# Optimization experiments

Hardware: AMD Instinct MI355X
Metric: run time of the kernel (lower is better)

Reference implementation:

```python
import jax, jax.numpy as jnp
import numpy as np
from jax import lax

KERNEL_SIZE = 2  # init kwarg erode_kernel


def _min_filter_same(x, k):
    """Separable k x k min-filter (erosion) over the last two dims of NCHW x,
    SAME output size, out-of-bounds padded with +inf (matches cv2.erode's
    default border value, which never wins the min)."""
    inf = jnp.asarray(jnp.inf, x.dtype)
    # rows pass then cols pass; square min-filter is separable
    y = lax.reduce_window(x, inf, lax.min,
                          window_dimensions=(1, 1, k, 1),
                          window_strides=(1, 1, 1, 1),
                          padding='SAME')
    y = lax.reduce_window(y, inf, lax.min,
                          window_dimensions=(1, 1, 1, k),
                          window_strides=(1, 1, 1, 1),
                          padding='SAME')
    return y


def setup_inputs() -> dict:
    key = jax.random.key(0)
    x = jax.random.normal(key, (32, 3, 512, 512), dtype=jnp.float32)
    return {"x": x, "l": 1, "gpu": 0}


def reference(x, l, gpu):
    # iterations_times = 4 * (l + 2 - 1); erosion window grows by 2*iters
    iterations_times = 4 * (l + 1)
    k = KERNEL_SIZE + 2 * iterations_times  # 18 for l=1
    # original: tensor2pil(e * 0.5 + 0.5) -> cv2.erode -> pil2tensor ([0,1])
    # (uint8 quantization of the PIL round-trip is omitted; same min-filter math)
    y = x * 0.5 + 0.5
    y = _min_filter_same(y, k)
    return y
```

## Files before the change

### kernel.cpp

```cpp
#include <hip/hip_runtime.h>


#define IMG_H 512
#define IMG_W 512
#define RLO 8

__device__ __forceinline__ float finf() { return __int_as_float(0x7f800000); }


__global__ __launch_bounds__(256, 4)
void erode_fused_22187801051678(const float* __restrict__ in,
                                float* __restrict__ out) {
    __shared__ float B[32][145];
    __shared__ float Bo[32][129];

    const int tid = threadIdx.x;
    const int w0 = blockIdx.x * 128;
    const int h0 = blockIdx.y * 32;
    const size_t plane = (size_t)blockIdx.z * (IMG_H * IMG_W);

    for (int u = tid; u < 290; u += 256) {
        int col, seg;
        if (u < 145) { col = u;       seg = 0; }
        else         { col = u - 145; seg = 1; }
        const int gw  = w0 - RLO + col;
        const bool wok = (unsigned)gw < (unsigned)IMG_W;
        const int ghb = h0 - RLO + seg * 16;

        float x[33];
#pragma unroll
        for (int i = 0; i < 33; ++i) {
            const int gh = ghb + i;
            float v = finf();
            if (wok && (unsigned)gh < (unsigned)IMG_H)
                v = in[plane + (size_t)gh * IMG_W + gw];
            x[i] = v;
        }
        float p[32];
#pragma unroll
        for (int i = 0; i < 32; ++i) p[i] = fminf(x[i], x[i + 1]);
        float q[30];
#pragma unroll
        for (int i = 0; i < 30; ++i) q[i] = fminf(p[i], p[i + 2]);
#pragma unroll
        for (int j = 0; j < 16; ++j) {
            float m = fminf(fminf(q[j], q[j + 4]), fminf(q[j + 8], q[j + 12]));
            m = fminf(m, p[j + 16]);
            B[seg * 16 + j][col] = m;
        }
    }
    __syncthreads();

    {
        const int r  = tid & 31;
        const int c8 = tid >> 5;
        float y[33];
#pragma unroll
        for (int i = 0; i < 33; ++i) y[i] = B[r][c8 * 16 + i];
        float p[32];
#pragma unroll
        for (int i = 0; i < 32; ++i) p[i] = fminf(y[i], y[i + 1]);
        float q[30];
#pragma unroll
        for (int i = 0; i < 30; ++i) q[i] = fminf(p[i], p[i + 2]);
#pragma unroll
        for (int j = 0; j < 16; ++j) {
            float m = fminf(fminf(q[j], q[j + 4]), fminf(q[j + 8], q[j + 12]));
            m = fminf(m, p[j + 16]);
            Bo[r][c8 * 16 + j] = m * 0.5f + 0.5f;
        }
    }
    __syncthreads();

#pragma unroll
    for (int t = 0; t < 16; ++t) {
        const int idx = t * 256 + tid;
        const int r = idx >> 7;
        const int c = idx & 127;
        out[plane + (size_t)(h0 + r) * IMG_W + (w0 + c)] = Bo[r][c];
    }
}

extern "C" void kernel_launch(void* const* d_in, const int* in_sizes, int n_in,
                              void* d_out, int out_size, void* d_ws, size_t ws_size,
                              hipStream_t stream) {
    const float* x = (const float*)d_in[0];
    float* out = (float*)d_out;
    const int planes = in_sizes[0] / (IMG_H * IMG_W);
    dim3 grid(IMG_W / 128, IMG_H / 32, planes);
    erode_fused_22187801051678<<<grid, dim3(256), 0, stream>>>(x, out);
}
```

Baseline: 185.8 us.

## Swap pass order to horizontal-first with float4 loads and vectorized column stores

```diff
diff --git a/kernel.cpp b/kernel.cpp
--- a/kernel.cpp
+++ b/kernel.cpp
@@ -1,83 +1,96 @@
 #include <hip/hip_runtime.h>
 
 
-#define IMG_H 512
-#define IMG_W 512
-#define RLO 8
+#define IMG 512
 
-__device__ __forceinline__ float finf() { return __int_as_float(0x7f800000); }
-
+__device__ __forceinline__ float4 f4min(float4 a, float4 b) {
+    return make_float4(fminf(a.x, b.x), fminf(a.y, b.y),
+                       fminf(a.z, b.z), fminf(a.w, b.w));
+}
 
 __global__ __launch_bounds__(256, 4)
 void erode_fused_22187801051678(const float* __restrict__ in,
                                 float* __restrict__ out) {
-    __shared__ float B[32][145];
-    __shared__ float Bo[32][129];
+    __shared__ float4 H[49][33];
 
     const int tid = threadIdx.x;
     const int w0 = blockIdx.x * 128;
     const int h0 = blockIdx.y * 32;
-    const size_t plane = (size_t)blockIdx.z * (IMG_H * IMG_W);
+    const size_t plane = (size_t)blockIdx.z * (size_t)(IMG * IMG);
 
-    for (int u = tid; u < 290; u += 256) {
-        int col, seg;
-        if (u < 145) { col = u;       seg = 0; }
-        else         { col = u - 145; seg = 1; }
-        const int gw  = w0 - RLO + col;
-        const bool wok = (unsigned)gw < (unsigned)IMG_W;
-        const int ghb = h0 - RLO + seg * 16;
+    for (int u = tid; u < 392; u += 256) {
+        const int chunk = u & 7;
+        const int row   = u >> 3;
+        const int gh    = h0 - 8 + row;
+        const int cbase = w0 + 16 * chunk - 8;
 
-        float x[33];
+        float y[36];
+        if ((unsigned)gh < (unsigned)IMG) {
+            const float* rp = in + plane + (size_t)gh * IMG;
 #pragma unroll
-        for (int i = 0; i < 33; ++i) {
-            const int gh = ghb + i;
-            float v = finf();
-            if (wok && (unsigned)gh < (unsigned)IMG_H)
-                v = in[plane + (size_t)gh * IMG_W + gw];
-            x[i] = v;
+            for (int g = 0; g < 9; ++g) {
+                const int c0 = cbase + 4 * g;
+                float4 v;
+                if ((unsigned)c0 < (unsigned)IMG)
+                    v = *reinterpret_cast<const float4*>(rp + c0);
+                else
+                    v = make_float4(__builtin_inff(), __builtin_inff(),
+                                    __builtin_inff(), __builtin_inff());
+                y[4 * g + 0] = v.x; y[4 * g + 1] = v.y;
+                y[4 * g + 2] = v.z; y[4 * g + 3] = v.w;
+            }
+        } else {
+#pragma unroll
+            for (int i = 0; i < 36; ++i) y[i] = __builtin_inff();
         }
-        float p[32];
-#pragma unroll
-        for (int i = 0; i < 32; ++i) p[i] = fminf(x[i], x[i + 1]);
-        float q[30];
-#pragma unroll
-        for (int i = 0; i < 30; ++i) q[i] = fminf(p[i], p[i + 2]);
-#pragma unroll
-        for (int j = 0; j < 16; ++j) {
-            float m = fminf(fminf(q[j], q[j + 4]), fminf(q[j + 8], q[j + 12]));
-            m = fminf(m, p[j + 16]);
-            B[seg * 16 + j][col] = m;
-        }
-    }
-    __syncthreads();
 
-    {
-        const int r  = tid & 31;
-        const int c8 = tid >> 5;
-        float y[33];
-#pragma unroll
-        for (int i = 0; i < 33; ++i) y[i] = B[r][c8 * 16 + i];
         float p[32];
 #pragma unroll
         for (int i = 0; i < 32; ++i) p[i] = fminf(y[i], y[i + 1]);
         float q[30];
 #pragma unroll
         for (int i = 0; i < 30; ++i) q[i] = fminf(p[i], p[i + 2]);
+        float o[16];
 #pragma unroll
         for (int j = 0; j < 16; ++j) {
             float m = fminf(fminf(q[j], q[j + 4]), fminf(q[j + 8], q[j + 12]));
-            m = fminf(m, p[j + 16]);
-            Bo[r][c8 * 16 + j] = m * 0.5f + 0.5f;
+            o[j] = fminf(m, p[j + 16]);
         }
+#pragma unroll
+        for (int jj = 0; jj < 4; ++jj)
+            H[row][4 * chunk + jj] =
+                make_float4(o[4 * jj], o[4 * jj + 1], o[4 * jj + 2], o[4 * jj + 3]);
     }
     __syncthreads();
 
+    {
+        const int c   = tid & 31;
+        const int seg = tid >> 5;
+        const int rb  = seg * 4;
+
+        float4 x0 = H[rb + 0][c];
+        float4 x1 = H[rb + 1][c];
+        float4 x2 = H[rb + 2][c];
+        float4 cm = H[rb + 3][c];
 #pragma unroll
-    for (int t = 0; t < 16; ++t) {
-        const int idx = t * 256 + tid;
-        const int r = idx >> 7;
-        const int c = idx & 127;
-        out[plane + (size_t)(h0 + r) * IMG_W + (w0 + c)] = Bo[r][c];
+        for (int k = 4; k <= 17; ++k) cm = f4min(cm, H[rb + k][c]);
+        float4 x18 = H[rb + 18][c];
+        float4 x19 = H[rb + 19][c];
+        float4 x20 = H[rb + 20][c];
+
+        float4 o0 = f4min(f4min(x0, x1), f4min(x2, cm));
+        float4 o1 = f4min(f4min(x1, x2), f4min(cm, x18));
+        float4 o2 = f4min(x2, f4min(cm, f4min(x18, x19)));
+        float4 o3 = f4min(f4min(cm, x18), f4min(x19, x20));
+
+        float* op = out + plane + (size_t)(h0 + rb) * IMG + (w0 + 4 * c);
+#define AFF4(v) make_float4(v.x * 0.5f + 0.5f, v.y * 0.5f + 0.5f, \
+                            v.z * 0.5f + 0.5f, v.w * 0.5f + 0.5f)
+        *reinterpret_cast<float4*>(op)            = AFF4(o0);
+        *reinterpret_cast<float4*>(op + IMG)      = AFF4(o1);
+        *reinterpret_cast<float4*>(op + 2 * IMG)  = AFF4(o2);
+        *reinterpret_cast<float4*>(op + 3 * IMG)  = AFF4(o3);
+#undef AFF4
     }
 }
 
@@ -86,7 +99,7 @@
                               hipStream_t stream) {
     const float* x = (const float*)d_in[0];
     float* out = (float*)d_out;
-    const int planes = in_sizes[0] / (IMG_H * IMG_W);
-    dim3 grid(IMG_W / 128, IMG_H / 32, planes);
+    const int planes = in_sizes[0] / (IMG * IMG);
+    dim3 grid(IMG / 128, IMG / 32, planes);
     erode_fused_22187801051678<<<grid, dim3(256), 0, stream>>>(x, out);
 }
```

New measurement: 206.7 us. 11.2% more time.
